# Kernel tuning notes

Hardware: AMD Instinct MI355X
Metric: run time of the kernel (lower is better)

## Reference

```python
import jax, jax.numpy as jnp
import numpy as np

N_HEAD = 4
HEAD_DIM = 32
D_MODEL = 128
NEG_BIG = -1.0e9  # note: source uses (mask-1)*(-1e9), reproduced faithfully
LN_EPS = 1e-05


def _layer_norm(x, gain, bias):
    mean = jnp.mean(x, axis=-1, keepdims=True)
    var = jnp.mean(jnp.square(x - mean), axis=-1, keepdims=True)
    return gain * (x - mean) / jnp.sqrt(var + LN_EPS) + bias


def setup_inputs() -> dict:
    key = jax.random.key(0)
    ks = jax.random.split(key, 6)
    L, S, D = 8, 2048, D_MODEL
    x = jax.random.normal(ks[0], (L, S, D), dtype=jnp.float32)
    mask = jnp.ones((L, S), dtype=jnp.int32)
    qkv_w = jax.random.normal(ks[1], (D, 3 * D), dtype=jnp.float32) * (1.0 / np.sqrt(D))
    out_w = jax.random.normal(ks[2], (D, D), dtype=jnp.float32) * (1.0 / np.sqrt(D))
    w1 = jax.random.normal(ks[3], (D, 384), dtype=jnp.float32) * (1.0 / np.sqrt(D))
    b1 = jnp.zeros((384,), dtype=jnp.float32)
    w2 = jax.random.normal(ks[4], (384, D), dtype=jnp.float32) * (1.0 / np.sqrt(384))
    b2 = jnp.zeros((D,), dtype=jnp.float32)
    g1 = jnp.ones((D,), dtype=jnp.float32)
    be1 = jnp.zeros((D,), dtype=jnp.float32)
    g2 = jnp.ones((D,), dtype=jnp.float32)
    be2 = jnp.zeros((D,), dtype=jnp.float32)
    return {"x": x, "mask": mask, "qkv_w": qkv_w, "out_w": out_w,
            "w1": w1, "b1": b1, "w2": w2, "b2": b2,
            "g1": g1, "be1": be1, "g2": g2, "be2": be2}


def reference(x, mask, qkv_w, out_w, w1, b1, w2, b2, g1, be1, g2, be2):
    # x: [L, S, D] -- the python list axis of the original module is L (each element batch=1)
    L, S, D = x.shape
    H, hd = N_HEAD, HEAD_DIM
    m = mask.astype(jnp.float32)  # [L, S]

    # QKV projection (single shared weight, split into q/k/v)
    qkv = jnp.einsum('lsd,de->lse', x, qkv_w)  # [L, S, 3D]
    q, k, v = jnp.split(qkv, 3, axis=-1)
    q = q.reshape(L, S, H, hd).transpose(0, 2, 1, 3)  # [L, H, S, hd]
    k = k.reshape(L, S, H, hd).transpose(0, 2, 1, 3)
    v = v.reshape(L, S, H, hd).transpose(0, 2, 1, 3)

    scale = 1.0 / np.sqrt(D // H)
    scores = jnp.einsum('lhqd,lhkd->lhqk', q, k) * scale  # [L, H, S, S]

    # outer-product padding mask, faithful to source: amask*scores + (amask-1)*(-1e9)
    amask = (m[:, None, :, None] * m[:, None, None, :])  # [L, 1, S, S]
    masked = amask * scores + (amask - 1.0) * NEG_BIG
    attn = jax.nn.softmax(masked, axis=-1)

    ctx = jnp.einsum('lhqk,lhkd->lhqd', attn, v)  # [L, H, S, hd]
    ctx = ctx.transpose(0, 2, 1, 3).reshape(L, S, D)
    attn_out = jnp.einsum('lsd,de->lse', ctx, out_w)  # output projection

    # residual + LN1 (dropout rate 0.0 -> identity)
    h = _layer_norm(attn_out + x, g1, be1)

    # FFN: Dense(384, relu) -> Dense(128, relu)
    ff = jax.nn.relu(jnp.einsum('lsd,df->lsf', h, w1) + b1)
    ff = jax.nn.relu(jnp.einsum('lsf,fd->lsd', ff, w2) + b2)

    # residual + LN2
    out = _layer_norm(ff + h, g2, be2)
    return out
```

## Files before the change

kernel.cpp:

```cpp
#include <hip/hip_runtime.h>
#include <hip/hip_bf16.h>

typedef __attribute__((ext_vector_type(8))) short bf16x8;
typedef __attribute__((ext_vector_type(4))) float f32x4;
typedef unsigned short u16;
typedef unsigned int u32;

__device__ __forceinline__ u32 bfr(float x) {
  u32 u = __float_as_uint(x);
  return (u + 0x7fffu + ((u >> 16) & 1u)) >> 16;
}
__device__ __forceinline__ u32 pk2(float lo, float hi) {
  return bfr(lo) | (bfr(hi) << 16);
}
__device__ __forceinline__ u32 cvtpk(float lo, float hi) {
  u32 r;
  asm("v_cvt_pk_bf16_f32 %0, %1, %2" : "=v"(r) : "v"(lo), "v"(hi));
  return r;
}

__device__ __forceinline__ f32x4 mfma16(bf16x8 a, bf16x8 b, f32x4 c) {
  return __builtin_amdgcn_mfma_f32_16x16x32_bf16(a, b, c, 0, 0, 0);
}

__global__ __launch_bounds__(256) void prep_weights(
    const float* __restrict__ qkv_w, const float* __restrict__ out_w,
    const float* __restrict__ w1, const float* __restrict__ w2,
    u16* __restrict__ qkvT, u16* __restrict__ outT,
    u16* __restrict__ w1T, u16* __restrict__ w2T) {
  int idx = blockIdx.x * 256 + threadIdx.x;
  if (idx < 49152) {
    int n = idx >> 7, k = idx & 127;
    qkvT[idx] = (u16)bfr(qkv_w[k * 384 + n]);
  } else if (idx < 49152 + 16384) {
    int i = idx - 49152;
    int n = i >> 7, k = i & 127;
    outT[i] = (u16)bfr(out_w[k * 128 + n]);
  } else if (idx < 49152 + 16384 + 49152) {
    int i = idx - 49152 - 16384;
    int n = i >> 7, k = i & 127;
    w1T[i] = (u16)bfr(w1[k * 384 + n]);
  } else if (idx < 163840) {
    int i = idx - 49152 - 16384 - 49152;
    int n = i / 384, k = i - n * 384;
    w2T[i] = (u16)bfr(w2[k * 128 + n]);
  }
}

__global__ __launch_bounds__(256) void prep_x(const float* __restrict__ x,
                                              u16* __restrict__ xb) {
  int idx = blockIdx.x * 256 + threadIdx.x;
  const float4* p = (const float4*)(x + (size_t)idx * 8);
  float4 a = p[0], b = p[1];
  uint4 w = {pk2(a.x, a.y), pk2(a.z, a.w), pk2(b.x, b.y), pk2(b.z, b.w)};
  *(uint4*)(xb + (size_t)idx * 8) = w;
}

__global__ __launch_bounds__(256) void mask_flag(const int* __restrict__ mask,
                                                 int* __restrict__ flag) {
  __shared__ int wbad[4];
  int l = blockIdx.x;
  int bad = 0;
  for (int i = threadIdx.x; i < 2048; i += 256)
    bad |= (mask[l * 2048 + i] != 1);
  unsigned long long b = __ballot(bad != 0);
  if ((threadIdx.x & 63) == 0) wbad[threadIdx.x >> 6] = (b != 0ULL) ? 1 : 0;
  __syncthreads();
  if (threadIdx.x == 0)
    flag[l] = (wbad[0] | wbad[1] | wbad[2] | wbad[3]) ? 0 : 1;
}

template <int K, int N, int EPI>
__global__ __launch_bounds__(256) void gemm_bf16(
    const u16* __restrict__ A, const u16* __restrict__ WT,
    const float* __restrict__ bias,
    u16* __restrict__ O0, u16* __restrict__ O1, u16* __restrict__ O2) {
  __shared__ u16 lds_a[64 * 136];
  __shared__ u16 lds_b[64 * 136];
  const int m0 = blockIdx.x * 64, n0 = blockIdx.y * 64;
  const int tid = threadIdx.x, lane = tid & 63, wv = tid >> 6;
  const int wm = wv >> 1, wn = wv & 1, c = lane & 15, g = lane >> 4;

  f32x4 acc[2][2] = {};
  for (int kt = 0; kt < K / 128; ++kt) {
    if (kt) __syncthreads();
    for (int i = tid; i < 1024; i += 256) {
      int row = i >> 4, cc = (i & 15) * 8;
      *(uint4*)(&lds_a[row * 136 + cc]) =
          *(const uint4*)(A + (size_t)(m0 + row) * K + kt * 128 + cc);
      *(uint4*)(&lds_b[row * 136 + cc]) =
          *(const uint4*)(WT + (size_t)(n0 + row) * K + kt * 128 + cc);
    }
    __syncthreads();
#pragma unroll
    for (int ks = 0; ks < 4; ++ks) {
      bf16x8 a0 = *(bf16x8*)(&lds_a[(wm * 32 + c) * 136 + ks * 32 + 8 * g]);
      bf16x8 a1 = *(bf16x8*)(&lds_a[(wm * 32 + 16 + c) * 136 + ks * 32 + 8 * g]);
      bf16x8 b0 = *(bf16x8*)(&lds_b[(wn * 32 + c) * 136 + ks * 32 + 8 * g]);
      bf16x8 b1 = *(bf16x8*)(&lds_b[(wn * 32 + 16 + c) * 136 + ks * 32 + 8 * g]);
      acc[0][0] = mfma16(a0, b0, acc[0][0]);
      acc[0][1] = mfma16(a0, b1, acc[0][1]);
      acc[1][0] = mfma16(a1, b0, acc[1][0]);
      acc[1][1] = mfma16(a1, b1, acc[1][1]);
    }
  }
#pragma unroll
  for (int mi = 0; mi < 2; ++mi)
#pragma unroll
    for (int ni = 0; ni < 2; ++ni) {
      const int n = n0 + wn * 32 + ni * 16 + c;
      const int mb = m0 + wm * 32 + mi * 16 + 4 * g;
      if constexpr (EPI == 2) {
        float bv = bias[n];
#pragma unroll
        for (int r = 0; r < 4; ++r)
          O0[(size_t)(mb + r) * N + n] =
              (u16)bfr(fmaxf(acc[mi][ni][r] + bv, 0.f));
      } else {
        const int reg = n >> 7, hh = (n >> 5) & 3, d = n & 31;
        const int l = mb >> 11, s = mb & 2047;
        const size_t lh = (size_t)l * 4 + hh;
        if (reg == 0) {
#pragma unroll
          for (int r = 0; r < 4; ++r)
            O0[(lh * 2048 + s + r) * 32 + d] =
                (u16)bfr(acc[mi][ni][r] * 0.17677669529663687f);
        } else if (reg == 1) {
#pragma unroll
          for (int r = 0; r < 4; ++r)
            O1[(lh * 2048 + s + r) * 32 + d] = (u16)bfr(acc[mi][ni][r]);
        } else {
          uint2 w = {pk2(acc[mi][ni][0], acc[mi][ni][1]),
                     pk2(acc[mi][ni][2], acc[mi][ni][3])};
          *(uint2*)(O2 + (lh * 32 + d) * 2048 + s) = w;
        }
      }
    }
}

template <int K, bool RELU>
__global__ __launch_bounds__(256) void gemm_ln(
    const u16* __restrict__ A, const u16* __restrict__ WT,
    const float* __restrict__ bias, const float* __restrict__ resid,
    const float* __restrict__ gain, const float* __restrict__ lnb,
    float* __restrict__ outf, u16* __restrict__ outb) {
  __shared__ u16 lds_a[64 * 136];
  __shared__ u16 lds_b[128 * 136];
  const int m0 = blockIdx.x * 64;
  const int tid = threadIdx.x, lane = tid & 63, wv = tid >> 6;
  const int c = lane & 15, g = lane >> 4;

  f32x4 acc[8] = {};
  for (int kt = 0; kt < K / 128; ++kt) {
    if (kt) __syncthreads();
    for (int i = tid; i < 1024; i += 256) {
      int row = i >> 4, cc = (i & 15) * 8;
      *(uint4*)(&lds_a[row * 136 + cc]) =
          *(const uint4*)(A + (size_t)(m0 + row) * K + kt * 128 + cc);
    }
    for (int i = tid; i < 2048; i += 256) {
      int row = i >> 4, cc = (i & 15) * 8;
      *(uint4*)(&lds_b[row * 136 + cc]) =
          *(const uint4*)(WT + (size_t)row * K + kt * 128 + cc);
    }
    __syncthreads();
#pragma unroll
    for (int ks = 0; ks < 4; ++ks) {
      bf16x8 a = *(bf16x8*)(&lds_a[(wv * 16 + c) * 136 + ks * 32 + 8 * g]);
#pragma unroll
      for (int ni = 0; ni < 8; ++ni) {
        bf16x8 b = *(bf16x8*)(&lds_b[(ni * 16 + c) * 136 + ks * 32 + 8 * g]);
        acc[ni] = mfma16(a, b, acc[ni]);
      }
    }
  }
  const int rbase = m0 + wv * 16 + 4 * g;
  float gv[8], lb[8], bv[8];
#pragma unroll
  for (int ni = 0; ni < 8; ++ni) {
    gv[ni] = gain[ni * 16 + c];
    lb[ni] = lnb[ni * 16 + c];
    if constexpr (RELU) bv[ni] = bias[ni * 16 + c];
  }
  float t[8][4];
  float sum[4] = {0.f, 0.f, 0.f, 0.f}, sq[4] = {0.f, 0.f, 0.f, 0.f};
#pragma unroll
  for (int ni = 0; ni < 8; ++ni) {
#pragma unroll
    for (int r = 0; r < 4; ++r) {
      float v = acc[ni][r];
      if constexpr (RELU) v = fmaxf(v + bv[ni], 0.f);
      v += resid[(size_t)(rbase + r) * 128 + ni * 16 + c];
      t[ni][r] = v;
      sum[r] += v;
      sq[r] += v * v;
    }
  }
#pragma unroll
  for (int off = 1; off < 16; off <<= 1) {
#pragma unroll
    for (int r = 0; r < 4; ++r) {
      sum[r] += __shfl_xor(sum[r], off);
      sq[r] += __shfl_xor(sq[r], off);
    }
  }
#pragma unroll
  for (int r = 0; r < 4; ++r) {
    float mean = sum[r] * (1.0f / 128.0f);
    float var = sq[r] * (1.0f / 128.0f) - mean * mean;
    float inv = rsqrtf(var + 1e-5f);
#pragma unroll
    for (int ni = 0; ni < 8; ++ni) {
      float o = gv[ni] * (t[ni][r] - mean) * inv + lb[ni];
      outf[(size_t)(rbase + r) * 128 + ni * 16 + c] = o;
      if (outb) outb[(size_t)(rbase + r) * 128 + ni * 16 + c] = (u16)bfr(o);
    }
  }
}

__global__ __launch_bounds__(256) void attn4(
    const u16* __restrict__ Qs, const u16* __restrict__ Kb,
    const u16* __restrict__ Vt, const int* __restrict__ mask,
    const int* __restrict__ mflag, u16* __restrict__ ctx) {
  __shared__ u16 lds_k[2][64 * 40];
  __shared__ u16 lds_vt[2][32 * 72];
  __shared__ u16 lds_p[4][16 * 72];
  __shared__ float lds_mk[2][64];

  const int bid = blockIdx.x;
  const int qt = bid & 31, lh = bid >> 5;
  const int tid = threadIdx.x, lane = tid & 63, wv = tid >> 6;
  const int c = lane & 15, g = lane >> 4;
  const int tok0 = (lh >> 2) * 2048;
  const int h = lh & 3;
  const int allone = mflag[lh >> 2];

  const int qrow = qt * 64 + wv * 16 + c;
  const bf16x8 qf = *(const bf16x8*)(Qs + ((size_t)lh * 2048 + qrow) * 32 + 8 * g);
  const float mq = allone ? 1.0f : (float)mask[tok0 + qrow];

  const int kr_ = tid & 63, kc_ = tid >> 6;
  const int vr_ = tid >> 3, vc_ = tid & 7;
  const u16* kbase = Kb + ((size_t)lh * 2048) * 32 + kr_ * 32 + kc_ * 8;
  const u16* vbase = Vt + ((size_t)lh * 32 + vr_) * 2048 + vc_ * 8;

  uint4 krg, vrg;
  float mkv = 0.f;
  auto issue = [&](int kt0) {
    krg = *(const uint4*)(kbase + (size_t)kt0 * 32);
    vrg = *(const uint4*)(vbase + kt0);
    if (!allone && tid < 64) mkv = (float)mask[tok0 + kt0 + tid];
  };
  auto commit = [&](int buf) {
    *(uint4*)(&lds_k[buf][kr_ * 40 + kc_ * 8]) = krg;
    *(uint4*)(&lds_vt[buf][vr_ * 72 + vc_ * 8]) = vrg;
    if (!allone && tid < 64) lds_mk[buf][tid] = mkv;
  };

  issue(0);
  commit(0);
  __syncthreads();

  f32x4 acc0 = {0.f, 0.f, 0.f, 0.f}, acc1 = {0.f, 0.f, 0.f, 0.f};
  float m_run = -1e30f, lsum = 0.f;
  const f32x4 zf = {0.f, 0.f, 0.f, 0.f};

  for (int t = 0; t < 32; ++t) {
    const int cur = t & 1;
    if (t < 31) issue((t + 1) * 64);

    f32x4 s[4];
#pragma unroll
    for (int j = 0; j < 4; ++j) {
      bf16x8 a = *(bf16x8*)(&lds_k[cur][(16 * j + c) * 40 + 8 * g]);
      s[j] = mfma16(a, qf, zf);
    }
    float sv[16];
    if (allone) {
#pragma unroll
      for (int j = 0; j < 4; ++j)
#pragma unroll
        for (int r = 0; r < 4; ++r) sv[4 * j + r] = s[j][r];
    } else {
#pragma unroll
      for (int j = 0; j < 4; ++j) {
        float4 mk4 = *(float4*)(&lds_mk[cur][16 * j + 4 * g]);
        const float* mkp = (const float*)&mk4;
#pragma unroll
        for (int r = 0; r < 4; ++r) {
          float am = mq * mkp[r];
          sv[4 * j + r] = am * s[j][r] + (am - 1.0f) * (-1e9f);
        }
      }
    }
    float tmax = sv[0];
#pragma unroll
    for (int i = 1; i < 16; ++i) tmax = fmaxf(tmax, sv[i]);
    tmax = fmaxf(tmax, __shfl_xor(tmax, 16));
    tmax = fmaxf(tmax, __shfl_xor(tmax, 32));
    if (!__all(tmax <= m_run + 8.0f)) {
      float mnew = fmaxf(m_run, tmax);
      float corr = __expf(m_run - mnew);
      m_run = mnew;
      lsum *= corr;
      acc0 *= corr;
      acc1 *= corr;
    }
    float p[16], psum = 0.f;
#pragma unroll
    for (int i = 0; i < 16; ++i) {
      p[i] = __expf(sv[i] - m_run);
      psum += p[i];
    }
    lsum += psum;
#pragma unroll
    for (int j = 0; j < 4; ++j) {
      uint2 w = {cvtpk(p[4 * j], p[4 * j + 1]), cvtpk(p[4 * j + 2], p[4 * j + 3])};
      *(uint2*)(&lds_p[wv][c * 72 + 16 * j + 4 * g]) = w;
    }
    bf16x8 pb0 = *(bf16x8*)(&lds_p[wv][c * 72 + 8 * g]);
    bf16x8 pb1 = *(bf16x8*)(&lds_p[wv][c * 72 + 32 + 8 * g]);
    bf16x8 v00 = *(bf16x8*)(&lds_vt[cur][c * 72 + 8 * g]);
    bf16x8 v01 = *(bf16x8*)(&lds_vt[cur][c * 72 + 32 + 8 * g]);
    bf16x8 v10 = *(bf16x8*)(&lds_vt[cur][(16 + c) * 72 + 8 * g]);
    bf16x8 v11 = *(bf16x8*)(&lds_vt[cur][(16 + c) * 72 + 32 + 8 * g]);
    acc0 = mfma16(v00, pb0, acc0);
    acc0 = mfma16(v01, pb1, acc0);
    acc1 = mfma16(v10, pb0, acc1);
    acc1 = mfma16(v11, pb1, acc1);

    if (t < 31) commit(cur ^ 1);
    __syncthreads();
  }
  float lt = lsum;
  lt += __shfl_xor(lt, 16);
  lt += __shfl_xor(lt, 32);
  float inv = 1.0f / lt;
  u16* op = ctx + (size_t)(tok0 + qrow) * 128 + h * 32;
  uint2 o0 = {cvtpk(acc0[0] * inv, acc0[1] * inv),
              cvtpk(acc0[2] * inv, acc0[3] * inv)};
  uint2 o1 = {cvtpk(acc1[0] * inv, acc1[1] * inv),
              cvtpk(acc1[2] * inv, acc1[3] * inv)};
  *(uint2*)(op + 4 * g) = o0;
  *(uint2*)(op + 16 + 4 * g) = o1;
}

extern "C" void kernel_launch(void* const* d_in, const int* in_sizes, int n_in,
                              void* d_out, int out_size, void* d_ws,
                              size_t ws_size, hipStream_t stream) {
  (void)in_sizes; (void)n_in; (void)out_size; (void)ws_size;
  const float* x = (const float*)d_in[0];
  const int* mask = (const int*)d_in[1];
  const float* qkv_w = (const float*)d_in[2];
  const float* out_w = (const float*)d_in[3];
  const float* w1 = (const float*)d_in[4];
  const float* b1 = (const float*)d_in[5];
  const float* w2 = (const float*)d_in[6];
  const float* b2 = (const float*)d_in[7];
  const float* g1 = (const float*)d_in[8];
  const float* be1 = (const float*)d_in[9];
  const float* g2 = (const float*)d_in[10];
  const float* be2 = (const float*)d_in[11];
  float* out = (float*)d_out;

  char* ws = (char*)d_ws;
  const size_t MB = 1 << 20;
  u16* Qs = (u16*)(ws);
  u16* Kb = (u16*)(ws + 4 * MB);
  u16* Vt = (u16*)(ws + 8 * MB);
  u16* ff_bf = (u16*)(ws);
  u16* ctx_bf = (u16*)(ws + 12 * MB);
  float* h = (float*)(ws + 16 * MB);
  u16* h_bf = (u16*)(ws + 24 * MB);
  u16* x_bf = (u16*)(ws + 28 * MB);
  u16* qkvT = (u16*)(ws + 32 * MB);
  u16* outT = qkvT + 384 * 128;
  u16* w1T = outT + 128 * 128;
  u16* w2T = w1T + 384 * 128;
  int* mflag = (int*)(ws + 33 * MB);

  prep_weights<<<640, 256, 0, stream>>>(qkv_w, out_w, w1, w2, qkvT, outT, w1T, w2T);
  prep_x<<<1024, 256, 0, stream>>>(x, x_bf);
  mask_flag<<<8, 256, 0, stream>>>(mask, mflag);
  gemm_bf16<128, 384, 3><<<dim3(256, 6), 256, 0, stream>>>(
      x_bf, qkvT, nullptr, Qs, Kb, Vt);
  attn4<<<1024, 256, 0, stream>>>(Qs, Kb, Vt, mask, mflag, ctx_bf);
  gemm_ln<128, false><<<256, 256, 0, stream>>>(
      ctx_bf, outT, nullptr, x, g1, be1, h, h_bf);
  gemm_bf16<128, 384, 2><<<dim3(256, 6), 256, 0, stream>>>(
      h_bf, w1T, b1, ff_bf, nullptr, nullptr);
  gemm_ln<384, true><<<256, 256, 0, stream>>>(
      ff_bf, w2T, b2, h, g2, be2, out, nullptr);
}
```

Baseline: 103.9 us.

## Fuse prep kernels, convert x inside QKV GEMM, use exp2 softmax with MFMA row sums

Merges the weight-prep and mask-flag kernels into one launch, and drops the separate x-to-bf16 kernel by converting fp32 x while loading the QKV GEMM's A tile. In attention, log2(e) is folded into the Q scale so the all-ones-mask path uses raw exp2, with a higher rescale threshold. The row sum is computed by an extra MFMA against a ones vector instead of VALU adds and cross-lane shuffles. This trades fewer launches and fewer VALU ops for two extra MFMAs per tile. The row sum is now taken from bf16-rounded probabilities, and the QKV GEMM now reads fp32 x, doubling A-tile traffic since it is re-read across the 6 N-blocks.

```diff
diff --git a/kernel.cpp b/kernel.cpp
--- a/kernel.cpp
+++ b/kernel.cpp
@@ -18,17 +18,41 @@
   asm("v_cvt_pk_bf16_f32 %0, %1, %2" : "=v"(r) : "v"(lo), "v"(hi));
   return r;
 }
+__device__ __forceinline__ float exp2f_fast(float x) {
+#if __has_builtin(__builtin_amdgcn_exp2f)
+  return __builtin_amdgcn_exp2f(x);
+#else
+  float r;
+  asm("v_exp_f32 %0, %1" : "=v"(r) : "v"(x));
+  return r;
+#endif
+}
 
 __device__ __forceinline__ f32x4 mfma16(bf16x8 a, bf16x8 b, f32x4 c) {
   return __builtin_amdgcn_mfma_f32_16x16x32_bf16(a, b, c, 0, 0, 0);
 }
 
-__global__ __launch_bounds__(256) void prep_weights(
+__global__ __launch_bounds__(256) void prep_all(
     const float* __restrict__ qkv_w, const float* __restrict__ out_w,
     const float* __restrict__ w1, const float* __restrict__ w2,
+    const int* __restrict__ mask,
     u16* __restrict__ qkvT, u16* __restrict__ outT,
-    u16* __restrict__ w1T, u16* __restrict__ w2T) {
-  int idx = blockIdx.x * 256 + threadIdx.x;
+    u16* __restrict__ w1T, u16* __restrict__ w2T, int* __restrict__ flag) {
+  __shared__ int wbad[4];
+  int b = blockIdx.x;
+  if (b >= 640) {
+    int l = b - 640;
+    int bad = 0;
+    for (int i = threadIdx.x; i < 2048; i += 256)
+      bad |= (mask[l * 2048 + i] != 1);
+    unsigned long long bl = __ballot(bad != 0);
+    if ((threadIdx.x & 63) == 0) wbad[threadIdx.x >> 6] = (bl != 0ULL) ? 1 : 0;
+    __syncthreads();
+    if (threadIdx.x == 0)
+      flag[l] = (wbad[0] | wbad[1] | wbad[2] | wbad[3]) ? 0 : 1;
+    return;
+  }
+  int idx = b * 256 + threadIdx.x;
   if (idx < 49152) {
     int n = idx >> 7, k = idx & 127;
     qkvT[idx] = (u16)bfr(qkv_w[k * 384 + n]);
@@ -47,32 +71,9 @@
   }
 }
 
-__global__ __launch_bounds__(256) void prep_x(const float* __restrict__ x,
-                                              u16* __restrict__ xb) {
-  int idx = blockIdx.x * 256 + threadIdx.x;
-  const float4* p = (const float4*)(x + (size_t)idx * 8);
-  float4 a = p[0], b = p[1];
-  uint4 w = {pk2(a.x, a.y), pk2(a.z, a.w), pk2(b.x, b.y), pk2(b.z, b.w)};
-  *(uint4*)(xb + (size_t)idx * 8) = w;
-}
-
-__global__ __launch_bounds__(256) void mask_flag(const int* __restrict__ mask,
-                                                 int* __restrict__ flag) {
-  __shared__ int wbad[4];
-  int l = blockIdx.x;
-  int bad = 0;
-  for (int i = threadIdx.x; i < 2048; i += 256)
-    bad |= (mask[l * 2048 + i] != 1);
-  unsigned long long b = __ballot(bad != 0);
-  if ((threadIdx.x & 63) == 0) wbad[threadIdx.x >> 6] = (b != 0ULL) ? 1 : 0;
-  __syncthreads();
-  if (threadIdx.x == 0)
-    flag[l] = (wbad[0] | wbad[1] | wbad[2] | wbad[3]) ? 0 : 1;
-}
-
-template <int K, int N, int EPI>
+template <int K, int N, int EPI, bool CONVA>
 __global__ __launch_bounds__(256) void gemm_bf16(
-    const u16* __restrict__ A, const u16* __restrict__ WT,
+    const void* __restrict__ Av, const u16* __restrict__ WT,
     const float* __restrict__ bias,
     u16* __restrict__ O0, u16* __restrict__ O1, u16* __restrict__ O2) {
   __shared__ u16 lds_a[64 * 136];
@@ -86,8 +87,19 @@
     if (kt) __syncthreads();
     for (int i = tid; i < 1024; i += 256) {
       int row = i >> 4, cc = (i & 15) * 8;
-      *(uint4*)(&lds_a[row * 136 + cc]) =
-          *(const uint4*)(A + (size_t)(m0 + row) * K + kt * 128 + cc);
+      if constexpr (CONVA) {
+        const float* Af = (const float*)Av;
+        const float4* pa =
+            (const float4*)(Af + (size_t)(m0 + row) * K + kt * 128 + cc);
+        float4 v0 = pa[0], v1 = pa[1];
+        uint4 aw = {pk2(v0.x, v0.y), pk2(v0.z, v0.w), pk2(v1.x, v1.y),
+                    pk2(v1.z, v1.w)};
+        *(uint4*)(&lds_a[row * 136 + cc]) = aw;
+      } else {
+        const u16* Au = (const u16*)Av;
+        *(uint4*)(&lds_a[row * 136 + cc]) =
+            *(const uint4*)(Au + (size_t)(m0 + row) * K + kt * 128 + cc);
+      }
       *(uint4*)(&lds_b[row * 136 + cc]) =
           *(const uint4*)(WT + (size_t)(n0 + row) * K + kt * 128 + cc);
     }
@@ -123,8 +135,8 @@
         if (reg == 0) {
 #pragma unroll
           for (int r = 0; r < 4; ++r)
-            O0[(lh * 2048 + s + r) * 32 + d] =
-                (u16)bfr(acc[mi][ni][r] * 0.17677669529663687f);
+            O0[(lh * 2048 + s + r) * 32 + d] = (u16)bfr(
+                acc[mi][ni][r] * (0.17677669529663687f * 1.4426950408889634f));
         } else if (reg == 1) {
 #pragma unroll
           for (int r = 0; r < 4; ++r)
@@ -218,7 +230,7 @@
   }
 }
 
-__global__ __launch_bounds__(256) void attn4(
+__global__ __launch_bounds__(256) void attn5(
     const u16* __restrict__ Qs, const u16* __restrict__ Kb,
     const u16* __restrict__ Vt, const int* __restrict__ mask,
     const int* __restrict__ mflag, u16* __restrict__ ctx) {
@@ -262,8 +274,13 @@
   __syncthreads();
 
   f32x4 acc0 = {0.f, 0.f, 0.f, 0.f}, acc1 = {0.f, 0.f, 0.f, 0.f};
-  float m_run = -1e30f, lsum = 0.f;
+  f32x4 accL = {0.f, 0.f, 0.f, 0.f};
+  float m_run = -1e30f;
   const f32x4 zf = {0.f, 0.f, 0.f, 0.f};
+  const float thr = allone ? 11.542425f : 8.0f;
+  union { u32 u[4]; bf16x8 v; } onesU;
+  onesU.u[0] = onesU.u[1] = onesU.u[2] = onesU.u[3] = 0x3F803F80u;
+  const bf16x8 onesA = onesU.v;
 
   for (int t = 0; t < 32; ++t) {
     const int cur = t & 1;
@@ -288,8 +305,9 @@
         const float* mkp = (const float*)&mk4;
 #pragma unroll
         for (int r = 0; r < 4; ++r) {
+          float st = s[j][r] * 0.69314718055994531f;
           float am = mq * mkp[r];
-          sv[4 * j + r] = am * s[j][r] + (am - 1.0f) * (-1e9f);
+          sv[4 * j + r] = am * st + (am - 1.0f) * (-1e9f);
         }
       }
     }
@@ -298,21 +316,22 @@
     for (int i = 1; i < 16; ++i) tmax = fmaxf(tmax, sv[i]);
     tmax = fmaxf(tmax, __shfl_xor(tmax, 16));
     tmax = fmaxf(tmax, __shfl_xor(tmax, 32));
-    if (!__all(tmax <= m_run + 8.0f)) {
+    if (!__all(tmax <= m_run + thr)) {
       float mnew = fmaxf(m_run, tmax);
-      float corr = __expf(m_run - mnew);
+      float corr = allone ? exp2f_fast(m_run - mnew) : __expf(m_run - mnew);
       m_run = mnew;
-      lsum *= corr;
       acc0 *= corr;
       acc1 *= corr;
-    }
-    float p[16], psum = 0.f;
-#pragma unroll
-    for (int i = 0; i < 16; ++i) {
-      p[i] = __expf(sv[i] - m_run);
-      psum += p[i];
-    }
-    lsum += psum;
+      accL *= corr;
+    }
+    float p[16];
+    if (allone) {
+#pragma unroll
+      for (int i = 0; i < 16; ++i) p[i] = exp2f_fast(sv[i] - m_run);
+    } else {
+#pragma unroll
+      for (int i = 0; i < 16; ++i) p[i] = __expf(sv[i] - m_run);
+    }
 #pragma unroll
     for (int j = 0; j < 4; ++j) {
       uint2 w = {cvtpk(p[4 * j], p[4 * j + 1]), cvtpk(p[4 * j + 2], p[4 * j + 3])};
@@ -328,14 +347,13 @@
     acc0 = mfma16(v01, pb1, acc0);
     acc1 = mfma16(v10, pb0, acc1);
     acc1 = mfma16(v11, pb1, acc1);
+    accL = mfma16(onesA, pb0, accL);
+    accL = mfma16(onesA, pb1, accL);
 
     if (t < 31) commit(cur ^ 1);
     __syncthreads();
   }
-  float lt = lsum;
-  lt += __shfl_xor(lt, 16);
-  lt += __shfl_xor(lt, 32);
-  float inv = 1.0f / lt;
+  float inv = 1.0f / accL[0];
   u16* op = ctx + (size_t)(tok0 + qrow) * 128 + h * 32;
   uint2 o0 = {cvtpk(acc0[0] * inv, acc0[1] * inv),
               cvtpk(acc0[2] * inv, acc0[3] * inv)};
@@ -372,23 +390,21 @@
   u16* ctx_bf = (u16*)(ws + 12 * MB);
   float* h = (float*)(ws + 16 * MB);
   u16* h_bf = (u16*)(ws + 24 * MB);
-  u16* x_bf = (u16*)(ws + 28 * MB);
   u16* qkvT = (u16*)(ws + 32 * MB);
   u16* outT = qkvT + 384 * 128;
   u16* w1T = outT + 128 * 128;
   u16* w2T = w1T + 384 * 128;
   int* mflag = (int*)(ws + 33 * MB);
 
-  prep_weights<<<640, 256, 0, stream>>>(qkv_w, out_w, w1, w2, qkvT, outT, w1T, w2T);
-  prep_x<<<1024, 256, 0, stream>>>(x, x_bf);
-  mask_flag<<<8, 256, 0, stream>>>(mask, mflag);
-  gemm_bf16<128, 384, 3><<<dim3(256, 6), 256, 0, stream>>>(
-      x_bf, qkvT, nullptr, Qs, Kb, Vt);
-  attn4<<<1024, 256, 0, stream>>>(Qs, Kb, Vt, mask, mflag, ctx_bf);
+  prep_all<<<648, 256, 0, stream>>>(qkv_w, out_w, w1, w2, mask, qkvT, outT,
+                                    w1T, w2T, mflag);
+  gemm_bf16<128, 384, 3, true><<<dim3(256, 6), 256, 0, stream>>>(
+      (const void*)x, qkvT, nullptr, Qs, Kb, Vt);
+  attn5<<<1024, 256, 0, stream>>>(Qs, Kb, Vt, mask, mflag, ctx_bf);
   gemm_ln<128, false><<<256, 256, 0, stream>>>(
       ctx_bf, outT, nullptr, x, g1, be1, h, h_bf);
-  gemm_bf16<128, 384, 2><<<dim3(256, 6), 256, 0, stream>>>(
-      h_bf, w1T, b1, ff_bf, nullptr, nullptr);
+  gemm_bf16<128, 384, 2, false><<<dim3(256, 6), 256, 0, stream>>>(
+      (const void*)h_bf, w1T, b1, ff_bf, nullptr, nullptr);
   gemm_ln<384, true><<<256, 256, 0, stream>>>(
       ff_bf, w2T, b2, h, g2, be2, out, nullptr);
 }
```

Result: no change. 105.9 us (+2.0%).
